# Optimization experiments

Hardware: AMD Instinct MI355X
Metric: run time of the kernel (lower is better)

The kernel has to match this reference:

```python
import jax, jax.numpy as jnp
import numpy as np

B, T, I, H = 512, 1024, 64, 128

def setup_inputs() -> dict:
    key = jax.random.key(0)
    ks = jax.random.split(key, 7)
    s_ih = 1.0 / np.sqrt(H)  # torch nn.RNN init scale (uniform +-1/sqrt(H)); use scaled normal for stability
    return {
        "x": jax.random.normal(ks[0], (B, T, I), dtype=jnp.float32),
        "W_ih": jax.random.uniform(ks[1], (H, I), minval=-s_ih, maxval=s_ih, dtype=jnp.float32),
        "W_hh": jax.random.uniform(ks[2], (H, H), minval=-s_ih, maxval=s_ih, dtype=jnp.float32),
        "b_ih": jax.random.uniform(ks[3], (H,), minval=-s_ih, maxval=s_ih, dtype=jnp.float32),
        "b_hh": jax.random.uniform(ks[4], (H,), minval=-s_ih, maxval=s_ih, dtype=jnp.float32),
        "fc_w": jax.random.uniform(ks[5], (1, H), minval=-s_ih, maxval=s_ih, dtype=jnp.float32),
        "fc_b": jax.random.uniform(ks[6], (1,), minval=-s_ih, maxval=s_ih, dtype=jnp.float32),
    }

def reference(x, W_ih, W_hh, b_ih, b_hh, fc_w, fc_b):
    # Precompute input projection for all timesteps in one big GEMM: [B,T,H]
    xp = jnp.einsum("bti,hi->bth", x, W_ih) + b_ih + b_hh
    h0 = jnp.zeros((x.shape[0], W_hh.shape[0]), dtype=x.dtype)

    def step(h, xp_t):
        h = jnp.tanh(xp_t + h @ W_hh.T)
        return h, None

    # scan over time axis; only the final hidden state is needed (out[:, -1, :])
    h_last, _ = jax.lax.scan(step, h0, jnp.swapaxes(xp, 0, 1))
    out = h_last @ fc_w.T + fc_b  # [B, 1]
    return jax.nn.sigmoid(out)
```

## Files before the change

### kernel.cpp

```cpp
#include <hip/hip_runtime.h>


#define Bsz 512
#define Tt  1024
#define Ii  64
#define Hh  128
constexpr int TC = 32;
constexpr int NT = 512;

__device__ __forceinline__ float fast_tanh(float x) {
    float t = __builtin_amdgcn_exp2f(x * 2.8853900817779268f);
    return 1.0f - 2.0f * __builtin_amdgcn_rcpf(t + 1.0f);
}

__device__ __forceinline__ float fast_sigmoid(float z) {
    float t = __builtin_amdgcn_exp2f(-z * 1.4426950408889634f);
    return __builtin_amdgcn_rcpf(1.0f + t);
}

__global__ __launch_bounds__(NT, 4)
void rnn_fused(const float* __restrict__ x,
               const float* __restrict__ W_ih,
               const float* __restrict__ W_hh,
               const float* __restrict__ b_ih,
               const float* __restrict__ b_hh,
               const float* __restrict__ fc_w,
               const float* __restrict__ fc_b,
               float* __restrict__ out)
{
    __shared__ float xs[2][TC * Ii];
    __shared__ float hbuf[2][Hh];
    __shared__ float wred[NT / 64];

    const int tid = threadIdx.x;
    const int j   = tid >> 2;
    const int kq  = tid & 3;
    const int row = blockIdx.x;
    const int rot = (2 * kq) & 7;

    float4 wih[4];
    {
        const float4* g = (const float4*)(W_ih + j * Ii + kq * 16);
        #pragma unroll
        for (int k = 0; k < 4; ++k) wih[k] = g[k];
    }
    float4 whh[8];
    {
        const float4* g = (const float4*)(W_hh + j * Hh + kq * 32);
        #pragma unroll
        for (int i = 0; i < 8; ++i) whh[i] = g[(i + rot) & 7];
    }
    const float bias = b_ih[j] + b_hh[j];

    if (kq == 0) hbuf[0][j] = 0.0f;

    const float4* xsrc = (const float4*)(x + (size_t)row * Tt * Ii);
    float4 pf = xsrc[tid];

    int   cur   = 0;
    float hlast = 0.0f;

    for (int t0 = 0; t0 < Tt; t0 += TC) {
        const int cbuf = (t0 / TC) & 1;
        ((float4*)xs[cbuf])[tid] = pf;
        if (t0 + TC < Tt) pf = xsrc[(t0 + TC) * (Ii / 4) + tid];
        __syncthreads();

        #pragma unroll 1
        for (int tt = 0; tt < TC; ++tt) {
            const float4* xv = (const float4*)(xs[cbuf] + tt * Ii) + kq * 4;
            const float4* hv = (const float4*)(hbuf[cur]) + kq * 8;

            float a0 = 0.f, a1 = 0.f, a2 = 0.f, a3 = 0.f;
            #pragma unroll
            for (int k = 0; k < 4; ++k) {
                float4 xx = xv[k]; float4 w = wih[k];
                a0 += xx.x * w.x; a1 += xx.y * w.y;
                a2 += xx.z * w.z; a3 += xx.w * w.w;
            }
            #pragma unroll
            for (int i = 0; i < 8; ++i) {
                float4 hh = hv[(i + rot) & 7];
                float4 w  = whh[i];
                a0 += hh.x * w.x; a1 += hh.y * w.y;
                a2 += hh.z * w.z; a3 += hh.w * w.w;
            }
            float p = (a0 + a1) + (a2 + a3);
            p += __shfl_xor(p, 1, 64);
            p += __shfl_xor(p, 2, 64);
            float z = p + bias;
            hlast = fast_tanh(z);
            if (kq == 0) hbuf[cur ^ 1][j] = hlast;
            __syncthreads();
            cur ^= 1;
        }
    }

    float partial = (kq == 0) ? fc_w[j] * hlast : 0.0f;
    #pragma unroll
    for (int off = 32; off > 0; off >>= 1)
        partial += __shfl_down(partial, off, 64);
    if ((tid & 63) == 0) wred[tid >> 6] = partial;
    __syncthreads();
    if (tid == 0) {
        float zz = fc_b[0];
        #pragma unroll
        for (int w = 0; w < NT / 64; ++w) zz += wred[w];
        out[row] = fast_sigmoid(zz);
    }
}

extern "C" void kernel_launch(void* const* d_in, const int* in_sizes, int n_in,
                              void* d_out, int out_size, void* d_ws, size_t ws_size,
                              hipStream_t stream) {
    const float* x    = (const float*)d_in[0];
    const float* W_ih = (const float*)d_in[1];
    const float* W_hh = (const float*)d_in[2];
    const float* b_ih = (const float*)d_in[3];
    const float* b_hh = (const float*)d_in[4];
    const float* fc_w = (const float*)d_in[5];
    const float* fc_b = (const float*)d_in[6];
    float* out = (float*)d_out;

    rnn_fused<<<Bsz, NT, 0, stream>>>(x, W_ih, W_hh, b_ih, b_hh, fc_w, fc_b, out);
}
```

Before: 700.7 us.

## Halve block size and compute two hidden units per thread in RNN step

Block size drops from 512 to 256 threads. Each thread now computes two hidden units, so each h vector read from LDS is reused for two weight rows and the per-step barrier spans 4 waves instead of 8. The aim is cheaper per-step synchronization and fewer LDS reads on the serial recurrence. In exchange it doubles per-thread work and register use (96 weight floats), and pins waves-per-EU to 2, which may limit latency hiding.

```diff
diff --git a/kernel.cpp b/kernel.cpp
--- a/kernel.cpp
+++ b/kernel.cpp
@@ -6,7 +6,7 @@
 #define Ii  64
 #define Hh  128
 constexpr int TC = 32;
-constexpr int NT = 512;
+constexpr int NT = 256;
 
 __device__ __forceinline__ float fast_tanh(float x) {
     float t = __builtin_amdgcn_exp2f(x * 2.8853900817779268f);
@@ -18,7 +18,7 @@
     return __builtin_amdgcn_rcpf(1.0f + t);
 }
 
-__global__ __launch_bounds__(NT, 4)
+__global__ __launch_bounds__(NT) __attribute__((amdgpu_waves_per_eu(2, 2)))
 void rnn_fused(const float* __restrict__ x,
                const float* __restrict__ W_ih,
                const float* __restrict__ W_hh,
@@ -33,80 +33,106 @@
     __shared__ float wred[NT / 64];
 
     const int tid = threadIdx.x;
-    const int j   = tid >> 2;
     const int kq  = tid & 3;
+    const int jg  = tid >> 2;
+    const int j0  = jg * 2, j1 = j0 + 1;
     const int row = blockIdx.x;
-    const int rot = (2 * kq) & 7;
+    const int rot = kq;
 
-    float4 wih[4];
+    float4 wih0[4], wih1[4];
     {
-        const float4* g = (const float4*)(W_ih + j * Ii + kq * 16);
+        const float4* g0 = (const float4*)(W_ih + j0 * Ii + kq * 16);
+        const float4* g1 = (const float4*)(W_ih + j1 * Ii + kq * 16);
         #pragma unroll
-        for (int k = 0; k < 4; ++k) wih[k] = g[k];
+        for (int k = 0; k < 4; ++k) { wih0[k] = g0[k]; wih1[k] = g1[k]; }
     }
-    float4 whh[8];
+    float4 whh0[8], whh1[8];
     {
-        const float4* g = (const float4*)(W_hh + j * Hh + kq * 32);
+        const float4* G0 = (const float4*)(W_hh + j0 * Hh + kq * 32);
+        const float4* G1 = (const float4*)(W_hh + j1 * Hh + kq * 32);
         #pragma unroll
-        for (int i = 0; i < 8; ++i) whh[i] = g[(i + rot) & 7];
+        for (int i = 0; i < 8; ++i) {
+            whh0[i] = G0[(i + rot) & 7];
+            whh1[i] = G1[(i + rot) & 7];
+        }
     }
-    const float bias = b_ih[j] + b_hh[j];
+    const float bias0 = b_ih[j0] + b_hh[j0];
+    const float bias1 = b_ih[j1] + b_hh[j1];
+    const float fw0 = fc_w[j0], fw1 = fc_w[j1];
 
-    if (kq == 0) hbuf[0][j] = 0.0f;
+    if (tid < Hh) hbuf[0][tid] = 0.0f;
 
     const float4* xsrc = (const float4*)(x + (size_t)row * Tt * Ii);
-    float4 pf = xsrc[tid];
+    float4 p0 = xsrc[tid];
+    float4 p1 = xsrc[tid + NT];
 
-    int   cur   = 0;
-    float hlast = 0.0f;
+    int   cur = 0;
+    float h0n = 0.0f, h1n = 0.0f;
 
     for (int t0 = 0; t0 < Tt; t0 += TC) {
         const int cbuf = (t0 / TC) & 1;
-        ((float4*)xs[cbuf])[tid] = pf;
-        if (t0 + TC < Tt) pf = xsrc[(t0 + TC) * (Ii / 4) + tid];
+        ((float4*)xs[cbuf])[tid]      = p0;
+        ((float4*)xs[cbuf])[tid + NT] = p1;
+        if (t0 + TC < Tt) {
+            const int base = (t0 + TC) * (Ii / 4);
+            p0 = xsrc[base + tid];
+            p1 = xsrc[base + tid + NT];
+        }
         __syncthreads();
 
-        #pragma unroll 1
+        #pragma unroll 2
         for (int tt = 0; tt < TC; ++tt) {
             const float4* xv = (const float4*)(xs[cbuf] + tt * Ii) + kq * 4;
             const float4* hv = (const float4*)(hbuf[cur]) + kq * 8;
 
-            float a0 = 0.f, a1 = 0.f, a2 = 0.f, a3 = 0.f;
+            float a00 = 0.f, a01 = 0.f, a02 = 0.f, a03 = 0.f;
+            float a10 = 0.f, a11 = 0.f, a12 = 0.f, a13 = 0.f;
             #pragma unroll
             for (int k = 0; k < 4; ++k) {
-                float4 xx = xv[k]; float4 w = wih[k];
-                a0 += xx.x * w.x; a1 += xx.y * w.y;
-                a2 += xx.z * w.z; a3 += xx.w * w.w;
+                float4 xx = xv[k];
+                float4 w0 = wih0[k], w1 = wih1[k];
+                a00 += xx.x * w0.x; a01 += xx.y * w0.y;
+                a02 += xx.z * w0.z; a03 += xx.w * w0.w;
+                a10 += xx.x * w1.x; a11 += xx.y * w1.y;
+                a12 += xx.z * w1.z; a13 += xx.w * w1.w;
             }
             #pragma unroll
             for (int i = 0; i < 8; ++i) {
                 float4 hh = hv[(i + rot) & 7];
-                float4 w  = whh[i];
-                a0 += hh.x * w.x; a1 += hh.y * w.y;
-                a2 += hh.z * w.z; a3 += hh.w * w.w;
+                float4 w0 = whh0[i], w1 = whh1[i];
+                a00 += hh.x * w0.x; a01 += hh.y * w0.y;
+                a02 += hh.z * w0.z; a03 += hh.w * w0.w;
+                a10 += hh.x * w1.x; a11 += hh.y * w1.y;
+                a12 += hh.z * w1.z; a13 += hh.w * w1.w;
             }
-            float p = (a0 + a1) + (a2 + a3);
-            p += __shfl_xor(p, 1, 64);
-            p += __shfl_xor(p, 2, 64);
-            float z = p + bias;
-            hlast = fast_tanh(z);
-            if (kq == 0) hbuf[cur ^ 1][j] = hlast;
+            float pp0 = (a00 + a01) + (a02 + a03);
+            float pp1 = (a10 + a11) + (a12 + a13);
+            pp0 += __shfl_xor(pp0, 1, 64);
+            pp0 += __shfl_xor(pp0, 2, 64);
+            pp1 += __shfl_xor(pp1, 1, 64);
+            pp1 += __shfl_xor(pp1, 2, 64);
+            h0n = fast_tanh(pp0 + bias0);
+            h1n = fast_tanh(pp1 + bias1);
+            if (kq == 0) {
+                float2 hw; hw.x = h0n; hw.y = h1n;
+                ((float2*)hbuf[cur ^ 1])[jg] = hw;
+            }
             __syncthreads();
             cur ^= 1;
         }
     }
 
-    float partial = (kq == 0) ? fc_w[j] * hlast : 0.0f;
+    float partial = (kq == 0) ? (fw0 * h0n + fw1 * h1n) : 0.0f;
     #pragma unroll
     for (int off = 32; off > 0; off >>= 1)
         partial += __shfl_down(partial, off, 64);
     if ((tid & 63) == 0) wred[tid >> 6] = partial;
     __syncthreads();
     if (tid == 0) {
-        float zz = fc_b[0];
+        float z = fc_b[0];
         #pragma unroll
-        for (int w = 0; w < NT / 64; ++w) zz += wred[w];
-        out[row] = fast_sigmoid(zz);
+        for (int w = 0; w < NT / 64; ++w) z += wred[w];
+        out[row] = fast_sigmoid(z);
     }
 }
 
```

After: 958.8 us. 1.37x slower.
